# Kernel optimization log

Measured on AMD Instinct MI355X. Metric: run time of the kernel, lower is better.

Reference implementation:

```python
import jax, jax.numpy as jnp
import numpy as np

DIM = 256
HEADS = 8
DIM_HEAD = 64
INNER = HEADS * DIM_HEAD  # 512
B, N = 4, 1024


def setup_inputs() -> dict:
    key = jax.random.key(0)
    ks = jax.random.split(key, 7)
    x = jax.random.normal(ks[0], (B, N, DIM), dtype=jnp.float32)
    attn_bias = jax.random.normal(ks[1], (B, HEADS, N, N), dtype=jnp.float32)
    s = 1.0 / np.sqrt(DIM)
    Wq = jax.random.normal(ks[2], (DIM, INNER), dtype=jnp.float32) * s
    Wkv = jax.random.normal(ks[3], (DIM, 2 * INNER), dtype=jnp.float32) * s
    # to_out initialized to zero in the torch module; use small random so output is non-trivial
    Wo = jax.random.normal(ks[4], (INNER, DIM), dtype=jnp.float32) * (1.0 / np.sqrt(INNER))
    bo = jnp.zeros((DIM,), dtype=jnp.float32)
    # gating initialized weight=0, bias=1 -> sigmoid(1); use small random weight + bias 1
    Wg = jax.random.normal(ks[5], (DIM, INNER), dtype=jnp.float32) * 0.02
    bg = jnp.ones((INNER,), dtype=jnp.float32)
    return {"x": x, "attn_bias": attn_bias, "Wq": Wq, "Wkv": Wkv,
            "Wo": Wo, "bo": bo, "Wg": Wg, "bg": bg}


def reference(x, attn_bias, Wq, Wkv, Wo, bo, Wg, bg):
    b, n, _ = x.shape
    scale = DIM_HEAD ** -0.5
    q = x @ Wq                                    # [b, n, inner]
    kv = x @ Wkv                                  # [b, n, 2*inner]
    k, v = jnp.split(kv, 2, axis=-1)
    def split_heads(t):
        return t.reshape(b, n, HEADS, DIM_HEAD).transpose(0, 2, 1, 3)  # [b,h,n,d]
    q, k, v = split_heads(q) * scale, split_heads(k), split_heads(v)
    dots = jnp.einsum('bhid,bhjd->bhij', q, k) + attn_bias
    # explicit max-subtract then softmax (matches original; numerically identical)
    attn = jax.nn.softmax(dots, axis=-1)
    out = jnp.einsum('bhij,bhjd->bhid', attn, v)  # [b,h,n,d]
    out = out.transpose(0, 2, 1, 3).reshape(b, n, INNER)
    gates = jax.nn.sigmoid(x @ Wg + bg)
    out = out * gates
    return out @ Wo + bo
```

## Files before the change

### kernel.cpp

```cpp
#include <hip/hip_runtime.h>

typedef unsigned short u16;
typedef unsigned int u32;
typedef __attribute__((ext_vector_type(8))) __bf16 bf16x8;
typedef __attribute__((ext_vector_type(4))) float floatx4;
typedef const __attribute__((address_space(1))) unsigned char glob_u8;
typedef __attribute__((address_space(3))) unsigned char lds_u8;

#define DEV __device__ __forceinline__

DEV u16 f2bf(float f) {
  u32 u = __builtin_bit_cast(u32, f);
  u = (u + 0x7fffu + ((u >> 16) & 1u)) >> 16;
  return (u16)u;
}
DEV float bf2f(u16 h) {
  u32 u = ((u32)h) << 16;
  return __builtin_bit_cast(float, u);
}
DEV floatx4 MFMA(bf16x8 a, bf16x8 b, floatx4 c) {
  return __builtin_amdgcn_mfma_f32_16x16x32_bf16(a, b, c, 0, 0, 0);
}

__global__ void convert_k(const float* __restrict__ x, const float* __restrict__ Wq,
                          const float* __restrict__ Wkv, const float* __restrict__ Wg,
                          const float* __restrict__ Wo,
                          u16* __restrict__ xb, u16* __restrict__ WcatT, u16* __restrict__ WoT) {
  int i = blockIdx.x * 256 + threadIdx.x;
  if (i < 1048576) { xb[i] = f2bf(x[i]); return; }
  i -= 1048576;
  if (i < 524288) {
    int n = i >> 8, kk = i & 255;
    float v;
    if (n < 512) v = Wq[kk * 512 + n];
    else if (n < 1536) v = Wkv[kk * 1024 + (n - 512)];
    else v = Wg[kk * 512 + (n - 1536)];
    WcatT[i] = f2bf(v);
    return;
  }
  i -= 524288;
  if (i < 131072) {
    int n = i >> 9, kk = i & 511;
    WoT[i] = f2bf(Wo[kk * 256 + n]);
  }
}

__global__ __launch_bounds__(256, 4) void gemm_qkvg(
    const u16* __restrict__ xb, const u16* __restrict__ WcatT, const float* __restrict__ bg,
    u16* __restrict__ qb, u16* __restrict__ kfrag, u16* __restrict__ vfrag, u16* __restrict__ gb) {
  __shared__ __attribute__((aligned(16))) u16 As[128 * 40];
  __shared__ __attribute__((aligned(16))) u16 Bs[64 * 40];
  const int tid = threadIdx.x;
  const int wave = tid >> 6, lane = tid & 63;
  const int lane15 = lane & 15, quad = lane >> 4;
  const int rm0 = blockIdx.x * 128;
  const int cn0 = blockIdx.y * 64;
  const int wm = (wave & 1) * 64, wn = (wave >> 1) * 32;
  const int rowA = tid >> 1, segA = (tid & 1) * 16;
  const int rowB = tid >> 2, segB = (tid & 3) * 8;
  floatx4 acc[4][2] = {};
  uint4 a0 = *(const uint4*)(xb + (rm0 + rowA) * 256 + segA);
  uint4 a1 = *(const uint4*)(xb + (rm0 + rowA) * 256 + segA + 8);
  uint4 b0 = *(const uint4*)(WcatT + (cn0 + rowB) * 256 + segB);
#pragma unroll 1
  for (int k0 = 0; k0 < 256; k0 += 32) {
    __syncthreads();
    *(uint4*)(As + rowA * 40 + segA) = a0;
    *(uint4*)(As + rowA * 40 + segA + 8) = a1;
    *(uint4*)(Bs + rowB * 40 + segB) = b0;
    __syncthreads();
    if (k0 < 224) {
      a0 = *(const uint4*)(xb + (rm0 + rowA) * 256 + k0 + 32 + segA);
      a1 = *(const uint4*)(xb + (rm0 + rowA) * 256 + k0 + 32 + segA + 8);
      b0 = *(const uint4*)(WcatT + (cn0 + rowB) * 256 + k0 + 32 + segB);
    }
    bf16x8 af[4], bfr[2];
#pragma unroll
    for (int mt = 0; mt < 4; ++mt) af[mt] = *(const bf16x8*)(As + (wm + mt * 16 + lane15) * 40 + quad * 8);
#pragma unroll
    for (int nt = 0; nt < 2; ++nt) bfr[nt] = *(const bf16x8*)(Bs + (wn + nt * 16 + lane15) * 40 + quad * 8);
#pragma unroll
    for (int mt = 0; mt < 4; ++mt)
#pragma unroll
      for (int nt = 0; nt < 2; ++nt)
        acc[mt][nt] = MFMA(af[mt], bfr[nt], acc[mt][nt]);
  }
#pragma unroll
  for (int mt = 0; mt < 4; ++mt)
#pragma unroll
    for (int nt = 0; nt < 2; ++nt)
#pragma unroll
      for (int r = 0; r < 4; ++r) {
        int row = rm0 + wm + mt * 16 + quad * 4 + r;
        int col = cn0 + wn + nt * 16 + lane15;
        float v = acc[mt][nt][r];
        int b = row >> 10, n = row & 1023;
        if (col < 512) {
          int h = col >> 6, d = col & 63;
          qb[((b * 8 + h) * 1024 + n) * 64 + d] = f2bf(v * 0.125f);
        } else if (col < 1024) {
          int c = col - 512, h = c >> 6, d = c & 63;
          int bh2 = b * 8 + h;
          int t = n >> 4, l15 = n & 15;
          int half = d >> 5, qd = (d >> 3) & 3, e = d & 7;
          kfrag[(size_t)bh2 * 65536 + t * 1024 + half * 512 + (qd * 16 + l15) * 8 + e] = f2bf(v);
        } else if (col < 1536) {
          int c = col - 1024, h = c >> 6, d = c & 63;
          int bh2 = b * 8 + h;
          int t64 = n >> 6, ck = (n >> 5) & 1, qd = (n >> 3) & 3, e = n & 7;
          int dt = d >> 4, l15 = d & 15;
          vfrag[(size_t)bh2 * 65536 + t64 * 4096 + dt * 1024 + ck * 512 + (qd * 16 + l15) * 8 + e] = f2bf(v);
        } else {
          int c = col - 1536;
          float g = 1.0f / (1.0f + __expf(-(v + bg[c])));
          gb[row * 512 + c] = f2bf(g);
        }
      }
}

__global__ __launch_bounds__(256, 2) void attn_k(
    const u16* __restrict__ qb, const u16* __restrict__ kfrag, const u16* __restrict__ vfrag,
    const float* __restrict__ bias, const u16* __restrict__ gb, u16* __restrict__ ogb) {
  __shared__ __attribute__((aligned(16))) u16 Kt[2][4096];
  __shared__ __attribute__((aligned(16))) u16 Vt[2][4096];
  __shared__ __attribute__((aligned(16))) float Bt[2][4096];
  __shared__ __attribute__((aligned(16))) u16 Ps[4 * 16 * 72];
  const int tid = threadIdx.x;
  const int wave = tid >> 6, lane = tid & 63;
  const int lane15 = lane & 15, quad = lane >> 4;
  const int bh = blockIdx.x;
  const int q0 = blockIdx.y * 64;

  bf16x8 qf0, qf1;
  {
    const u16* qrow = qb + ((size_t)(bh * 1024 + q0 + wave * 16 + lane15)) * 64 + quad * 8;
    qf0 = *(const bf16x8*)(qrow);
    qf1 = *(const bf16x8*)(qrow + 32);
  }
  bf16x8 ones;
#pragma unroll
  for (int e = 0; e < 8; ++e) ones[e] = __builtin_bit_cast(__bf16, (u16)0x3F80);

  floatx4 oacc[4] = {};
  floatx4 lacc = {};

  u16* Pw = Ps + wave * (16 * 72);
  const u16* kp = kfrag + (size_t)bh * 65536;
  const u16* vp = vfrag + (size_t)bh * 65536;

  auto stage = [&](int kt, int bufi) {
    const int kb0 = kt * 64;
    const u16* kS = kp + kb0 * 64;
    const u16* vS = vp + kb0 * 64;
#pragma unroll
    for (int c = 0; c < 2; ++c) {
      int ch = wave * 2 + c;
      __builtin_amdgcn_global_load_lds((glob_u8*)(kS + ch * 512 + lane * 8),
                                       (lds_u8*)(&Kt[bufi][ch * 512]), 16, 0, 0);
      __builtin_amdgcn_global_load_lds((glob_u8*)(vS + ch * 512 + lane * 8),
                                       (lds_u8*)(&Vt[bufi][ch * 512]), 16, 0, 0);
    }
#pragma unroll
    for (int c = 0; c < 4; ++c) {
      int ch = wave * 4 + c;
      const float* bS = bias + ((size_t)(bh * 1024 + q0 + ch * 4 + quad)) * 1024 + kb0 + lane15 * 4;
      __builtin_amdgcn_global_load_lds((glob_u8*)bS, (lds_u8*)(&Bt[bufi][ch * 256]), 16, 0, 0);
    }
  };

  stage(0, 0);
  __syncthreads();
  int cur = 0;
#pragma unroll 1
  for (int kt = 0; kt < 16; ++kt) {
    if (kt < 15) stage(kt + 1, cur ^ 1);
    const u16* Ktc = Kt[cur];
    const u16* Vtc = Vt[cur];
    const float* Btc = Bt[cur];
    floatx4 s[4];
#pragma unroll
    for (int j = 0; j < 4; ++j) {
      bf16x8 kf0 = *(const bf16x8*)(Ktc + j * 1024 + lane * 8);
      bf16x8 kf1 = *(const bf16x8*)(Ktc + j * 1024 + 512 + lane * 8);
      floatx4 z = {};
      z = MFMA(qf0, kf0, z);
      s[j] = MFMA(qf1, kf1, z);
    }
#pragma unroll
    for (int j = 0; j < 4; ++j)
#pragma unroll
      for (int r = 0; r < 4; ++r)
        s[j][r] = __expf(s[j][r] + Btc[(wave * 16 + quad * 4 + r) * 64 + j * 16 + lane15] - 8.0f);
#pragma unroll
    for (int j = 0; j < 4; ++j)
#pragma unroll
      for (int r = 0; r < 4; ++r)
        Pw[(quad * 4 + r) * 72 + j * 16 + lane15] = f2bf(s[j][r]);
    bf16x8 pf0 = *(const bf16x8*)(Pw + lane15 * 72 + quad * 8);
    bf16x8 pf1 = *(const bf16x8*)(Pw + lane15 * 72 + 32 + quad * 8);

    lacc = MFMA(pf0, ones, lacc);
    lacc = MFMA(pf1, ones, lacc);
#pragma unroll
    for (int dt = 0; dt < 4; ++dt) {
      bf16x8 vf0 = *(const bf16x8*)(Vtc + dt * 1024 + lane * 8);
      bf16x8 vf1 = *(const bf16x8*)(Vtc + dt * 1024 + 512 + lane * 8);
      oacc[dt] = MFMA(pf0, vf0, oacc[dt]);
      oacc[dt] = MFMA(pf1, vf1, oacc[dt]);
    }
    __syncthreads();
    cur ^= 1;
  }

  const int b = bh >> 3, h = bh & 7;
#pragma unroll
  for (int r = 0; r < 4; ++r) {
    int q = q0 + wave * 16 + quad * 4 + r;
    float inv = 1.0f / lacc[r];
    size_t base = ((size_t)(b * 1024 + q)) * 512 + h * 64;
#pragma unroll
    for (int dt = 0; dt < 4; ++dt) {
      size_t gi = base + dt * 16 + lane15;
      ogb[gi] = f2bf(oacc[dt][r] * inv * bf2f(gb[gi]));
    }
  }
}

__global__ __launch_bounds__(256, 4) void gemm_out_k(
    const u16* __restrict__ og, const u16* __restrict__ WoT,
    const float* __restrict__ bo, float* __restrict__ out) {
  __shared__ __attribute__((aligned(16))) u16 As[64 * 40];
  __shared__ __attribute__((aligned(16))) u16 Bs[64 * 40];
  const int tid = threadIdx.x;
  const int wave = tid >> 6, lane = tid & 63;
  const int lane15 = lane & 15, quad = lane >> 4;
  const int rm0 = blockIdx.x * 64;
  const int cn0 = blockIdx.y * 64;
  const int wm = (wave & 1) * 32, wn = (wave >> 1) * 32;
  const int rowA = tid >> 2, segA = (tid & 3) * 8;
  floatx4 acc[2][2] = {};
  uint4 a0 = *(const uint4*)(og + (rm0 + rowA) * 512 + segA);
  uint4 b0 = *(const uint4*)(WoT + (cn0 + rowA) * 512 + segA);
#pragma unroll 1
  for (int k0 = 0; k0 < 512; k0 += 32) {
    __syncthreads();
    *(uint4*)(As + rowA * 40 + segA) = a0;
    *(uint4*)(Bs + rowA * 40 + segA) = b0;
    __syncthreads();
    if (k0 < 480) {
      a0 = *(const uint4*)(og + (rm0 + rowA) * 512 + k0 + 32 + segA);
      b0 = *(const uint4*)(WoT + (cn0 + rowA) * 512 + k0 + 32 + segA);
    }
    bf16x8 af[2], bfr[2];
#pragma unroll
    for (int mt = 0; mt < 2; ++mt) af[mt] = *(const bf16x8*)(As + (wm + mt * 16 + lane15) * 40 + quad * 8);
#pragma unroll
    for (int nt = 0; nt < 2; ++nt) bfr[nt] = *(const bf16x8*)(Bs + (wn + nt * 16 + lane15) * 40 + quad * 8);
#pragma unroll
    for (int mt = 0; mt < 2; ++mt)
#pragma unroll
      for (int nt = 0; nt < 2; ++nt)
        acc[mt][nt] = MFMA(af[mt], bfr[nt], acc[mt][nt]);
  }
#pragma unroll
  for (int nt = 0; nt < 2; ++nt) {
    int col = cn0 + wn + nt * 16 + lane15;
    float bv = bo[col];
#pragma unroll
    for (int mt = 0; mt < 2; ++mt)
#pragma unroll
      for (int r = 0; r < 4; ++r) {
        int row = rm0 + wm + mt * 16 + quad * 4 + r;
        out[(size_t)row * 256 + col] = acc[mt][nt][r] + bv;
      }
  }
}

extern "C" void kernel_launch(void* const* d_in, const int* in_sizes, int n_in,
                              void* d_out, int out_size, void* d_ws, size_t ws_size,
                              hipStream_t stream) {
  const float* x = (const float*)d_in[0];
  const float* bias = (const float*)d_in[1];
  const float* Wq = (const float*)d_in[2];
  const float* Wkv = (const float*)d_in[3];
  const float* Wo = (const float*)d_in[4];
  const float* bo = (const float*)d_in[5];
  const float* Wg = (const float*)d_in[6];
  const float* bg = (const float*)d_in[7];
  float* out = (float*)d_out;
  char* ws = (char*)d_ws;
  u16* xb    = (u16*)(ws);
  u16* WcatT = (u16*)(ws + 2097152);
  u16* WoT   = (u16*)(ws + 3145728);
  u16* qb    = (u16*)(ws + 3407872);
  u16* kfrag = (u16*)(ws + 7602176);
  u16* vfrag = (u16*)(ws + 11796480);
  u16* gb    = (u16*)(ws + 15990784);
  u16* ogb   = (u16*)(ws + 20185088);

  convert_k<<<6656, 256, 0, stream>>>(x, Wq, Wkv, Wg, Wo, xb, WcatT, WoT);
  dim3 g1(32, 32);
  gemm_qkvg<<<g1, 256, 0, stream>>>(xb, WcatT, bg, qb, kfrag, vfrag, gb);
  dim3 g2(32, 16);
  attn_k<<<g2, 256, 0, stream>>>(qb, kfrag, vfrag, bias, gb, ogb);
  dim3 g3(64, 4);
  gemm_out_k<<<g3, 256, 0, stream>>>(ogb, WoT, bo, out);
}
```

Baseline: 252.6 us.

## Fuse four kernels into one persistent kernel with software grid barriers

Merges the conversion, QKV/gate GEMM, attention and output GEMM into a single 512-block kernel separated by atomic-counter grid barriers. Each stage maps its former grid onto the fixed block count: the QKV GEMM does two tiles per block, and the output GEMM uses smaller 32-row tiles. This removes the per-launch overheads and gaps between kernels. In exchange it adds barrier latency, forces all stages to share one occupancy and LDS footprint, adds a memset, and relies on all 512 blocks being co-resident; the barrier's spin guard can break out early and let blocks continue on unfinished data.

```diff
diff --git a/kernel.cpp b/kernel.cpp
--- a/kernel.cpp
+++ b/kernel.cpp
@@ -8,6 +8,7 @@
 typedef __attribute__((address_space(3))) unsigned char lds_u8;
 
 #define DEV __device__ __forceinline__
+#define NB 512u
 
 DEV u16 f2bf(float f) {
   u32 u = __builtin_bit_cast(u32, f);
@@ -22,257 +23,280 @@
   return __builtin_amdgcn_mfma_f32_16x16x32_bf16(a, b, c, 0, 0, 0);
 }
 
-__global__ void convert_k(const float* __restrict__ x, const float* __restrict__ Wq,
-                          const float* __restrict__ Wkv, const float* __restrict__ Wg,
-                          const float* __restrict__ Wo,
-                          u16* __restrict__ xb, u16* __restrict__ WcatT, u16* __restrict__ WoT) {
-  int i = blockIdx.x * 256 + threadIdx.x;
-  if (i < 1048576) { xb[i] = f2bf(x[i]); return; }
-  i -= 1048576;
-  if (i < 524288) {
-    int n = i >> 8, kk = i & 255;
-    float v;
-    if (n < 512) v = Wq[kk * 512 + n];
-    else if (n < 1536) v = Wkv[kk * 1024 + (n - 512)];
-    else v = Wg[kk * 512 + (n - 1536)];
-    WcatT[i] = f2bf(v);
-    return;
-  }
-  i -= 524288;
-  if (i < 131072) {
-    int n = i >> 9, kk = i & 511;
-    WoT[i] = f2bf(Wo[kk * 256 + n]);
-  }
-}
-
-__global__ __launch_bounds__(256, 4) void gemm_qkvg(
-    const u16* __restrict__ xb, const u16* __restrict__ WcatT, const float* __restrict__ bg,
-    u16* __restrict__ qb, u16* __restrict__ kfrag, u16* __restrict__ vfrag, u16* __restrict__ gb) {
-  __shared__ __attribute__((aligned(16))) u16 As[128 * 40];
-  __shared__ __attribute__((aligned(16))) u16 Bs[64 * 40];
+DEV void grid_sync(unsigned* cnt, unsigned* gen) {
+  __syncthreads();
+  if (threadIdx.x == 0) {
+    __threadfence();
+    unsigned g = __hip_atomic_load(gen, __ATOMIC_RELAXED, __HIP_MEMORY_SCOPE_AGENT);
+    unsigned a = __hip_atomic_fetch_add(cnt, 1u, __ATOMIC_ACQ_REL, __HIP_MEMORY_SCOPE_AGENT);
+    if (a == NB - 1u) {
+      __hip_atomic_store(cnt, 0u, __ATOMIC_RELAXED, __HIP_MEMORY_SCOPE_AGENT);
+      __hip_atomic_store(gen, g + 1u, __ATOMIC_RELEASE, __HIP_MEMORY_SCOPE_AGENT);
+    } else {
+      int guard = 0;
+      while (__hip_atomic_load(gen, __ATOMIC_ACQUIRE, __HIP_MEMORY_SCOPE_AGENT) == g) {
+        __builtin_amdgcn_s_sleep(4);
+        if (++guard > (1 << 22)) break;
+      }
+    }
+    __threadfence();
+  }
+  __syncthreads();
+}
+
+__global__ __launch_bounds__(256, 2) void fused_pipeline_k(
+    const float* __restrict__ x, const float* __restrict__ bias,
+    const float* __restrict__ Wq, const float* __restrict__ Wkv,
+    const float* __restrict__ Wo, const float* __restrict__ bo,
+    const float* __restrict__ Wg, const float* __restrict__ bg,
+    u16* __restrict__ xb, u16* __restrict__ WcatT, u16* __restrict__ WoT,
+    u16* __restrict__ qb, u16* __restrict__ kfrag, u16* __restrict__ vfrag,
+    u16* __restrict__ gb, u16* __restrict__ ogb, float* __restrict__ out,
+    unsigned* bar) {
+  __shared__ __attribute__((aligned(16))) unsigned char SM[74752];
   const int tid = threadIdx.x;
+  const int bid = blockIdx.x;
   const int wave = tid >> 6, lane = tid & 63;
   const int lane15 = lane & 15, quad = lane >> 4;
-  const int rm0 = blockIdx.x * 128;
-  const int cn0 = blockIdx.y * 64;
-  const int wm = (wave & 1) * 64, wn = (wave >> 1) * 32;
-  const int rowA = tid >> 1, segA = (tid & 1) * 16;
-  const int rowB = tid >> 2, segB = (tid & 3) * 8;
-  floatx4 acc[4][2] = {};
-  uint4 a0 = *(const uint4*)(xb + (rm0 + rowA) * 256 + segA);
-  uint4 a1 = *(const uint4*)(xb + (rm0 + rowA) * 256 + segA + 8);
-  uint4 b0 = *(const uint4*)(WcatT + (cn0 + rowB) * 256 + segB);
-#pragma unroll 1
-  for (int k0 = 0; k0 < 256; k0 += 32) {
+
+  {
+    const int i0 = bid * 256 + tid;
+#pragma unroll 1
+    for (int it = 0; it < 13; ++it) {
+      int i = i0 + it * 131072;
+      if (i < 1048576) { xb[i] = f2bf(x[i]); continue; }
+      int j = i - 1048576;
+      if (j < 524288) {
+        int n = j >> 8, kk = j & 255;
+        float v;
+        if (n < 512) v = Wq[kk * 512 + n];
+        else if (n < 1536) v = Wkv[kk * 1024 + (n - 512)];
+        else v = Wg[kk * 512 + (n - 1536)];
+        WcatT[j] = f2bf(v);
+        continue;
+      }
+      j -= 524288;
+      int n = j >> 9, kk = j & 511;
+      WoT[j] = f2bf(Wo[kk * 256 + n]);
+    }
+  }
+  grid_sync(bar, bar + 32);
+
+  {
+    u16* As = (u16*)SM;
+    u16* Bs = (u16*)(SM + 10240);
+    const int wm = (wave & 1) * 64, wn = (wave >> 1) * 32;
+    const int rowA = tid >> 1, segA = (tid & 1) * 16;
+    const int rowB = tid >> 2, segB = (tid & 3) * 8;
+#pragma unroll 1
+    for (int it = 0; it < 2; ++it) {
+      const int t = bid * 2 + it;
+      const int rm0 = (t & 31) * 128;
+      const int cn0 = (t >> 5) * 64;
+      floatx4 acc[4][2] = {};
+      uint4 a0 = *(const uint4*)(xb + (rm0 + rowA) * 256 + segA);
+      uint4 a1 = *(const uint4*)(xb + (rm0 + rowA) * 256 + segA + 8);
+      uint4 b0 = *(const uint4*)(WcatT + (cn0 + rowB) * 256 + segB);
+#pragma unroll 1
+      for (int k0 = 0; k0 < 256; k0 += 32) {
+        __syncthreads();
+        *(uint4*)(As + rowA * 40 + segA) = a0;
+        *(uint4*)(As + rowA * 40 + segA + 8) = a1;
+        *(uint4*)(Bs + rowB * 40 + segB) = b0;
+        __syncthreads();
+        if (k0 < 224) {
+          a0 = *(const uint4*)(xb + (rm0 + rowA) * 256 + k0 + 32 + segA);
+          a1 = *(const uint4*)(xb + (rm0 + rowA) * 256 + k0 + 32 + segA + 8);
+          b0 = *(const uint4*)(WcatT + (cn0 + rowB) * 256 + k0 + 32 + segB);
+        }
+        bf16x8 af[4], bfr[2];
+#pragma unroll
+        for (int mt = 0; mt < 4; ++mt) af[mt] = *(const bf16x8*)(As + (wm + mt * 16 + lane15) * 40 + quad * 8);
+#pragma unroll
+        for (int nt = 0; nt < 2; ++nt) bfr[nt] = *(const bf16x8*)(Bs + (wn + nt * 16 + lane15) * 40 + quad * 8);
+#pragma unroll
+        for (int mt = 0; mt < 4; ++mt)
+#pragma unroll
+          for (int nt = 0; nt < 2; ++nt)
+            acc[mt][nt] = MFMA(af[mt], bfr[nt], acc[mt][nt]);
+      }
+#pragma unroll
+      for (int mt = 0; mt < 4; ++mt)
+#pragma unroll
+        for (int nt = 0; nt < 2; ++nt)
+#pragma unroll
+          for (int r = 0; r < 4; ++r) {
+            int row = rm0 + wm + mt * 16 + quad * 4 + r;
+            int col = cn0 + wn + nt * 16 + lane15;
+            float v = acc[mt][nt][r];
+            int b = row >> 10, n = row & 1023;
+            if (col < 512) {
+              int h = col >> 6, d = col & 63;
+              qb[((b * 8 + h) * 1024 + n) * 64 + d] = f2bf(v * 0.125f);
+            } else if (col < 1024) {
+              int c = col - 512, h = c >> 6, d = c & 63;
+              int bh2 = b * 8 + h;
+              int tt = n >> 4, l15 = n & 15;
+              int half = d >> 5, qd = (d >> 3) & 3, e = d & 7;
+              kfrag[(size_t)bh2 * 65536 + tt * 1024 + half * 512 + (qd * 16 + l15) * 8 + e] = f2bf(v);
+            } else if (col < 1536) {
+              int c = col - 1024, h = c >> 6, d = c & 63;
+              int bh2 = b * 8 + h;
+              int t64 = n >> 6, ck = (n >> 5) & 1, qd = (n >> 3) & 3, e = n & 7;
+              int dt = d >> 4, l15 = d & 15;
+              vfrag[(size_t)bh2 * 65536 + t64 * 4096 + dt * 1024 + ck * 512 + (qd * 16 + l15) * 8 + e] = f2bf(v);
+            } else {
+              int c = col - 1536;
+              float g = 1.0f / (1.0f + __expf(-(v + bg[c])));
+              gb[row * 512 + c] = f2bf(g);
+            }
+          }
+    }
+  }
+  grid_sync(bar, bar + 32);
+
+  {
+    u16* KtL = (u16*)SM;
+    u16* VtL = (u16*)(SM + 16384);
+    float* BtL = (float*)(SM + 32768);
+    u16* PsL = (u16*)(SM + 65536);
+    const int bh = bid & 31;
+    const int q0 = (bid >> 5) * 64;
+
+    bf16x8 qf0, qf1;
+    {
+      const u16* qrow = qb + ((size_t)(bh * 1024 + q0 + wave * 16 + lane15)) * 64 + quad * 8;
+      qf0 = *(const bf16x8*)(qrow);
+      qf1 = *(const bf16x8*)(qrow + 32);
+    }
+    bf16x8 ones;
+#pragma unroll
+    for (int e = 0; e < 8; ++e) ones[e] = __builtin_bit_cast(__bf16, (u16)0x3F80);
+
+    floatx4 oacc[4] = {};
+    floatx4 lacc = {};
+
+    u16* Pw = PsL + wave * (16 * 72);
+    const u16* kp = kfrag + (size_t)bh * 65536;
+    const u16* vp = vfrag + (size_t)bh * 65536;
+
+    auto stage = [&](int kt, int bufi) {
+      const int kb0 = kt * 64;
+      const u16* kS = kp + kb0 * 64;
+      const u16* vS = vp + kb0 * 64;
+#pragma unroll
+      for (int c = 0; c < 2; ++c) {
+        int ch = wave * 2 + c;
+        __builtin_amdgcn_global_load_lds((glob_u8*)(kS + ch * 512 + lane * 8),
+                                         (lds_u8*)(KtL + bufi * 4096 + ch * 512), 16, 0, 0);
+        __builtin_amdgcn_global_load_lds((glob_u8*)(vS + ch * 512 + lane * 8),
+                                         (lds_u8*)(VtL + bufi * 4096 + ch * 512), 16, 0, 0);
+      }
+#pragma unroll
+      for (int c = 0; c < 4; ++c) {
+        int ch = wave * 4 + c;
+        const float* bS = bias + ((size_t)(bh * 1024 + q0 + ch * 4 + quad)) * 1024 + kb0 + lane15 * 4;
+        __builtin_amdgcn_global_load_lds((glob_u8*)bS, (lds_u8*)(BtL + bufi * 4096 + ch * 256), 16, 0, 0);
+      }
+    };
+
+    stage(0, 0);
     __syncthreads();
-    *(uint4*)(As + rowA * 40 + segA) = a0;
-    *(uint4*)(As + rowA * 40 + segA + 8) = a1;
-    *(uint4*)(Bs + rowB * 40 + segB) = b0;
-    __syncthreads();
-    if (k0 < 224) {
-      a0 = *(const uint4*)(xb + (rm0 + rowA) * 256 + k0 + 32 + segA);
-      a1 = *(const uint4*)(xb + (rm0 + rowA) * 256 + k0 + 32 + segA + 8);
-      b0 = *(const uint4*)(WcatT + (cn0 + rowB) * 256 + k0 + 32 + segB);
-    }
-    bf16x8 af[4], bfr[2];
-#pragma unroll
-    for (int mt = 0; mt < 4; ++mt) af[mt] = *(const bf16x8*)(As + (wm + mt * 16 + lane15) * 40 + quad * 8);
-#pragma unroll
-    for (int nt = 0; nt < 2; ++nt) bfr[nt] = *(const bf16x8*)(Bs + (wn + nt * 16 + lane15) * 40 + quad * 8);
-#pragma unroll
-    for (int mt = 0; mt < 4; ++mt)
-#pragma unroll
-      for (int nt = 0; nt < 2; ++nt)
-        acc[mt][nt] = MFMA(af[mt], bfr[nt], acc[mt][nt]);
-  }
-#pragma unroll
-  for (int mt = 0; mt < 4; ++mt)
-#pragma unroll
-    for (int nt = 0; nt < 2; ++nt)
+    int cur = 0;
+#pragma unroll 1
+    for (int kt = 0; kt < 16; ++kt) {
+      if (kt < 15) stage(kt + 1, cur ^ 1);
+      const u16* Ktc = KtL + cur * 4096;
+      const u16* Vtc = VtL + cur * 4096;
+      const float* Btc = BtL + cur * 4096;
+      floatx4 s[4];
+#pragma unroll
+      for (int j = 0; j < 4; ++j) {
+        bf16x8 kf0 = *(const bf16x8*)(Ktc + j * 1024 + lane * 8);
+        bf16x8 kf1 = *(const bf16x8*)(Ktc + j * 1024 + 512 + lane * 8);
+        floatx4 z = {};
+        z = MFMA(qf0, kf0, z);
+        s[j] = MFMA(qf1, kf1, z);
+      }
+#pragma unroll
+      for (int j = 0; j < 4; ++j)
+#pragma unroll
+        for (int r = 0; r < 4; ++r)
+          s[j][r] = __expf(s[j][r] + Btc[(wave * 16 + quad * 4 + r) * 64 + j * 16 + lane15] - 8.0f);
+#pragma unroll
+      for (int j = 0; j < 4; ++j)
+#pragma unroll
+        for (int r = 0; r < 4; ++r)
+          Pw[(quad * 4 + r) * 72 + j * 16 + lane15] = f2bf(s[j][r]);
+      bf16x8 pf0 = *(const bf16x8*)(Pw + lane15 * 72 + quad * 8);
+      bf16x8 pf1 = *(const bf16x8*)(Pw + lane15 * 72 + 32 + quad * 8);
+
+      lacc = MFMA(pf0, ones, lacc);
+      lacc = MFMA(pf1, ones, lacc);
+#pragma unroll
+      for (int dt = 0; dt < 4; ++dt) {
+        bf16x8 vf0 = *(const bf16x8*)(Vtc + dt * 1024 + lane * 8);
+        bf16x8 vf1 = *(const bf16x8*)(Vtc + dt * 1024 + 512 + lane * 8);
+        oacc[dt] = MFMA(pf0, vf0, oacc[dt]);
+        oacc[dt] = MFMA(pf1, vf1, oacc[dt]);
+      }
+      __syncthreads();
+      cur ^= 1;
+    }
+
+    const int b = bh >> 3, h = bh & 7;
+#pragma unroll
+    for (int r = 0; r < 4; ++r) {
+      int q = q0 + wave * 16 + quad * 4 + r;
+      float inv = 1.0f / lacc[r];
+      size_t base = ((size_t)(b * 1024 + q)) * 512 + h * 64;
+#pragma unroll
+      for (int dt = 0; dt < 4; ++dt) {
+        size_t gi = base + dt * 16 + lane15;
+        ogb[gi] = f2bf(oacc[dt][r] * inv * bf2f(gb[gi]));
+      }
+    }
+  }
+  grid_sync(bar, bar + 32);
+
+  {
+    u16* As = (u16*)SM;
+    u16* Bs = (u16*)(SM + 2560);
+    const int rm0 = (bid & 127) * 32;
+    const int cn0 = (bid >> 7) * 64;
+    const int wm = (wave & 1) * 16, wn = (wave >> 1) * 32;
+    const int rowA = tid >> 3, segA = (tid & 7) * 4;
+    const int rowB = tid >> 2, segB = (tid & 3) * 8;
+    floatx4 acc[2] = {};
+    uint2 a0 = *(const uint2*)(ogb + (rm0 + rowA) * 512 + segA);
+    uint4 b0 = *(const uint4*)(WoT + (cn0 + rowB) * 512 + segB);
+#pragma unroll 1
+    for (int k0 = 0; k0 < 512; k0 += 32) {
+      __syncthreads();
+      *(uint2*)(As + rowA * 40 + segA) = a0;
+      *(uint4*)(Bs + rowB * 40 + segB) = b0;
+      __syncthreads();
+      if (k0 < 480) {
+        a0 = *(const uint2*)(ogb + (rm0 + rowA) * 512 + k0 + 32 + segA);
+        b0 = *(const uint4*)(WoT + (cn0 + rowB) * 512 + k0 + 32 + segB);
+      }
+      bf16x8 af = *(const bf16x8*)(As + (wm + lane15) * 40 + quad * 8);
+      bf16x8 bfr[2];
+#pragma unroll
+      for (int nt = 0; nt < 2; ++nt) bfr[nt] = *(const bf16x8*)(Bs + (wn + nt * 16 + lane15) * 40 + quad * 8);
+#pragma unroll
+      for (int nt = 0; nt < 2; ++nt) acc[nt] = MFMA(af, bfr[nt], acc[nt]);
+    }
+#pragma unroll
+    for (int nt = 0; nt < 2; ++nt) {
+      int col = cn0 + wn + nt * 16 + lane15;
+      float bv = bo[col];
 #pragma unroll
       for (int r = 0; r < 4; ++r) {
-        int row = rm0 + wm + mt * 16 + quad * 4 + r;
-        int col = cn0 + wn + nt * 16 + lane15;
-        float v = acc[mt][nt][r];
-        int b = row >> 10, n = row & 1023;
-        if (col < 512) {
-          int h = col >> 6, d = col & 63;
-          qb[((b * 8 + h) * 1024 + n) * 64 + d] = f2bf(v * 0.125f);
-        } else if (col < 1024) {
-          int c = col - 512, h = c >> 6, d = c & 63;
-          int bh2 = b * 8 + h;
-          int t = n >> 4, l15 = n & 15;
-          int half = d >> 5, qd = (d >> 3) & 3, e = d & 7;
-          kfrag[(size_t)bh2 * 65536 + t * 1024 + half * 512 + (qd * 16 + l15) * 8 + e] = f2bf(v);
-        } else if (col < 1536) {
-          int c = col - 1024, h = c >> 6, d = c & 63;
-          int bh2 = b * 8 + h;
-          int t64 = n >> 6, ck = (n >> 5) & 1, qd = (n >> 3) & 3, e = n & 7;
-          int dt = d >> 4, l15 = d & 15;
-          vfrag[(size_t)bh2 * 65536 + t64 * 4096 + dt * 1024 + ck * 512 + (qd * 16 + l15) * 8 + e] = f2bf(v);
-        } else {
-          int c = col - 1536;
-          float g = 1.0f / (1.0f + __expf(-(v + bg[c])));
-          gb[row * 512 + c] = f2bf(g);
-        }
-      }
-}
-
-__global__ __launch_bounds__(256, 2) void attn_k(
-    const u16* __restrict__ qb, const u16* __restrict__ kfrag, const u16* __restrict__ vfrag,
-    const float* __restrict__ bias, const u16* __restrict__ gb, u16* __restrict__ ogb) {
-  __shared__ __attribute__((aligned(16))) u16 Kt[2][4096];
-  __shared__ __attribute__((aligned(16))) u16 Vt[2][4096];
-  __shared__ __attribute__((aligned(16))) float Bt[2][4096];
-  __shared__ __attribute__((aligned(16))) u16 Ps[4 * 16 * 72];
-  const int tid = threadIdx.x;
-  const int wave = tid >> 6, lane = tid & 63;
-  const int lane15 = lane & 15, quad = lane >> 4;
-  const int bh = blockIdx.x;
-  const int q0 = blockIdx.y * 64;
-
-  bf16x8 qf0, qf1;
-  {
-    const u16* qrow = qb + ((size_t)(bh * 1024 + q0 + wave * 16 + lane15)) * 64 + quad * 8;
-    qf0 = *(const bf16x8*)(qrow);
-    qf1 = *(const bf16x8*)(qrow + 32);
-  }
-  bf16x8 ones;
-#pragma unroll
-  for (int e = 0; e < 8; ++e) ones[e] = __builtin_bit_cast(__bf16, (u16)0x3F80);
-
-  floatx4 oacc[4] = {};
-  floatx4 lacc = {};
-
-  u16* Pw = Ps + wave * (16 * 72);
-  const u16* kp = kfrag + (size_t)bh * 65536;
-  const u16* vp = vfrag + (size_t)bh * 65536;
-
-  auto stage = [&](int kt, int bufi) {
-    const int kb0 = kt * 64;
-    const u16* kS = kp + kb0 * 64;
-    const u16* vS = vp + kb0 * 64;
-#pragma unroll
-    for (int c = 0; c < 2; ++c) {
-      int ch = wave * 2 + c;
-      __builtin_amdgcn_global_load_lds((glob_u8*)(kS + ch * 512 + lane * 8),
-                                       (lds_u8*)(&Kt[bufi][ch * 512]), 16, 0, 0);
-      __builtin_amdgcn_global_load_lds((glob_u8*)(vS + ch * 512 + lane * 8),
-                                       (lds_u8*)(&Vt[bufi][ch * 512]), 16, 0, 0);
-    }
-#pragma unroll
-    for (int c = 0; c < 4; ++c) {
-      int ch = wave * 4 + c;
-      const float* bS = bias + ((size_t)(bh * 1024 + q0 + ch * 4 + quad)) * 1024 + kb0 + lane15 * 4;
-      __builtin_amdgcn_global_load_lds((glob_u8*)bS, (lds_u8*)(&Bt[bufi][ch * 256]), 16, 0, 0);
-    }
-  };
-
-  stage(0, 0);
-  __syncthreads();
-  int cur = 0;
-#pragma unroll 1
-  for (int kt = 0; kt < 16; ++kt) {
-    if (kt < 15) stage(kt + 1, cur ^ 1);
-    const u16* Ktc = Kt[cur];
-    const u16* Vtc = Vt[cur];
-    const float* Btc = Bt[cur];
-    floatx4 s[4];
-#pragma unroll
-    for (int j = 0; j < 4; ++j) {
-      bf16x8 kf0 = *(const bf16x8*)(Ktc + j * 1024 + lane * 8);
-      bf16x8 kf1 = *(const bf16x8*)(Ktc + j * 1024 + 512 + lane * 8);
-      floatx4 z = {};
-      z = MFMA(qf0, kf0, z);
-      s[j] = MFMA(qf1, kf1, z);
-    }
-#pragma unroll
-    for (int j = 0; j < 4; ++j)
-#pragma unroll
-      for (int r = 0; r < 4; ++r)
-        s[j][r] = __expf(s[j][r] + Btc[(wave * 16 + quad * 4 + r) * 64 + j * 16 + lane15] - 8.0f);
-#pragma unroll
-    for (int j = 0; j < 4; ++j)
-#pragma unroll
-      for (int r = 0; r < 4; ++r)
-        Pw[(quad * 4 + r) * 72 + j * 16 + lane15] = f2bf(s[j][r]);
-    bf16x8 pf0 = *(const bf16x8*)(Pw + lane15 * 72 + quad * 8);
-    bf16x8 pf1 = *(const bf16x8*)(Pw + lane15 * 72 + 32 + quad * 8);
-
-    lacc = MFMA(pf0, ones, lacc);
-    lacc = MFMA(pf1, ones, lacc);
-#pragma unroll
-    for (int dt = 0; dt < 4; ++dt) {
-      bf16x8 vf0 = *(const bf16x8*)(Vtc + dt * 1024 + lane * 8);
-      bf16x8 vf1 = *(const bf16x8*)(Vtc + dt * 1024 + 512 + lane * 8);
-      oacc[dt] = MFMA(pf0, vf0, oacc[dt]);
-      oacc[dt] = MFMA(pf1, vf1, oacc[dt]);
-    }
-    __syncthreads();
-    cur ^= 1;
-  }
-
-  const int b = bh >> 3, h = bh & 7;
-#pragma unroll
-  for (int r = 0; r < 4; ++r) {
-    int q = q0 + wave * 16 + quad * 4 + r;
-    float inv = 1.0f / lacc[r];
-    size_t base = ((size_t)(b * 1024 + q)) * 512 + h * 64;
-#pragma unroll
-    for (int dt = 0; dt < 4; ++dt) {
-      size_t gi = base + dt * 16 + lane15;
-      ogb[gi] = f2bf(oacc[dt][r] * inv * bf2f(gb[gi]));
-    }
-  }
-}
-
-__global__ __launch_bounds__(256, 4) void gemm_out_k(
-    const u16* __restrict__ og, const u16* __restrict__ WoT,
-    const float* __restrict__ bo, float* __restrict__ out) {
-  __shared__ __attribute__((aligned(16))) u16 As[64 * 40];
-  __shared__ __attribute__((aligned(16))) u16 Bs[64 * 40];
-  const int tid = threadIdx.x;
-  const int wave = tid >> 6, lane = tid & 63;
-  const int lane15 = lane & 15, quad = lane >> 4;
-  const int rm0 = blockIdx.x * 64;
-  const int cn0 = blockIdx.y * 64;
-  const int wm = (wave & 1) * 32, wn = (wave >> 1) * 32;
-  const int rowA = tid >> 2, segA = (tid & 3) * 8;
-  floatx4 acc[2][2] = {};
-  uint4 a0 = *(const uint4*)(og + (rm0 + rowA) * 512 + segA);
-  uint4 b0 = *(const uint4*)(WoT + (cn0 + rowA) * 512 + segA);
-#pragma unroll 1
-  for (int k0 = 0; k0 < 512; k0 += 32) {
-    __syncthreads();
-    *(uint4*)(As + rowA * 40 + segA) = a0;
-    *(uint4*)(Bs + rowA * 40 + segA) = b0;
-    __syncthreads();
-    if (k0 < 480) {
-      a0 = *(const uint4*)(og + (rm0 + rowA) * 512 + k0 + 32 + segA);
-      b0 = *(const uint4*)(WoT + (cn0 + rowA) * 512 + k0 + 32 + segA);
-    }
-    bf16x8 af[2], bfr[2];
-#pragma unroll
-    for (int mt = 0; mt < 2; ++mt) af[mt] = *(const bf16x8*)(As + (wm + mt * 16 + lane15) * 40 + quad * 8);
-#pragma unroll
-    for (int nt = 0; nt < 2; ++nt) bfr[nt] = *(const bf16x8*)(Bs + (wn + nt * 16 + lane15) * 40 + quad * 8);
-#pragma unroll
-    for (int mt = 0; mt < 2; ++mt)
-#pragma unroll
-      for (int nt = 0; nt < 2; ++nt)
-        acc[mt][nt] = MFMA(af[mt], bfr[nt], acc[mt][nt]);
-  }
-#pragma unroll
-  for (int nt = 0; nt < 2; ++nt) {
-    int col = cn0 + wn + nt * 16 + lane15;
-    float bv = bo[col];
-#pragma unroll
-    for (int mt = 0; mt < 2; ++mt)
-#pragma unroll
-      for (int r = 0; r < 4; ++r) {
-        int row = rm0 + wm + mt * 16 + quad * 4 + r;
-        out[(size_t)row * 256 + col] = acc[mt][nt][r] + bv;
-      }
+        int row = rm0 + wm + quad * 4 + r;
+        out[(size_t)row * 256 + col] = acc[nt][r] + bv;
+      }
+    }
   }
 }
 
@@ -297,12 +321,10 @@
   u16* vfrag = (u16*)(ws + 11796480);
   u16* gb    = (u16*)(ws + 15990784);
   u16* ogb   = (u16*)(ws + 20185088);
-
-  convert_k<<<6656, 256, 0, stream>>>(x, Wq, Wkv, Wg, Wo, xb, WcatT, WoT);
-  dim3 g1(32, 32);
-  gemm_qkvg<<<g1, 256, 0, stream>>>(xb, WcatT, bg, qb, kfrag, vfrag, gb);
-  dim3 g2(32, 16);
-  attn_k<<<g2, 256, 0, stream>>>(qb, kfrag, vfrag, bias, gb, ogb);
-  dim3 g3(64, 4);
-  gemm_out_k<<<g3, 256, 0, stream>>>(ogb, WoT, bo, out);
-}
+  unsigned* bar = (unsigned*)(ws + 24379392);
+
+  hipMemsetAsync(bar, 0, 256, stream);
+  fused_pipeline_k<<<512, 256, 0, stream>>>(x, bias, Wq, Wkv, Wo, bo, Wg, bg,
+                                            xb, WcatT, WoT, qb, kfrag, vfrag,
+                                            gb, ogb, out, bar);
+}
```

Result: slower. 536.9 us (+112.5%).
